# Optimization experiments

Hardware: AMD Instinct MI355X
Metric: run time of the kernel (lower is better)

## Reference

```python
import jax, jax.numpy as jnp
import numpy as np

N = 50000
E = 1600000


def gcn_conv(x, W, b, src, dst, edge_weight):
    # PyG GCNConv(normalize=False): h = x @ W.T; msg_e = h[src_e] * w_e;
    # out_i = sum_{e: dst_e = i} msg_e + bias
    h = x @ W.T                                   # [N, C_out]
    msg = h[src]                                  # [E, C_out]
    if edge_weight is not None:
        msg = msg * edge_weight[:, None]
    agg = jax.ops.segment_sum(msg, dst, num_segments=N)  # [N, C_out]
    return agg + b


def batchnorm_eval(x, gamma, beta, mean, var, eps=1e-5):
    inv = gamma * jax.lax.rsqrt(var + eps)
    return (x - mean) * inv + beta


def setup_inputs() -> dict:
    key = jax.random.key(0)
    ks = jax.random.split(key, 16)
    d = {}
    d["x"] = jax.random.normal(ks[0], (N, 128), dtype=jnp.float32)
    d["edge_index"] = jax.random.randint(ks[1], (2, E), 0, N, dtype=jnp.int64)
    d["edge_attr"] = jax.random.uniform(ks[2], (E, 8), dtype=jnp.float32)
    # layer 1: 128 -> 256, layer 2: 256 -> 256, layer 3: 256 -> 256
    s1 = 1.0 / np.sqrt(128.0)
    s2 = 1.0 / np.sqrt(256.0)
    d["W1"] = jax.random.uniform(ks[3], (256, 128), jnp.float32, -s1, s1)
    d["b1"] = jnp.zeros((256,), jnp.float32)
    d["g1"] = jnp.ones((256,), jnp.float32)
    d["beta1"] = jnp.zeros((256,), jnp.float32)
    d["m1"] = jax.random.normal(ks[4], (256,), jnp.float32) * 0.1
    d["v1"] = jax.random.uniform(ks[5], (256,), jnp.float32, minval=0.5, maxval=1.5)
    d["W2"] = jax.random.uniform(ks[6], (256, 256), jnp.float32, -s2, s2)
    d["b2"] = jnp.zeros((256,), jnp.float32)
    d["g2"] = jnp.ones((256,), jnp.float32)
    d["beta2"] = jnp.zeros((256,), jnp.float32)
    d["m2"] = jax.random.normal(ks[7], (256,), jnp.float32) * 0.1
    d["v2"] = jax.random.uniform(ks[8], (256,), jnp.float32, minval=0.5, maxval=1.5)
    d["W3"] = jax.random.uniform(ks[9], (256, 256), jnp.float32, -s2, s2)
    d["b3"] = jnp.zeros((256,), jnp.float32)
    return d


def reference(x, edge_index, edge_attr, W1, b1, g1, beta1, m1, v1,
              W2, b2, g2, beta2, m2, v2, W3, b3):
    src, dst = edge_index[0], edge_index[1]
    ew = jnp.mean(edge_attr, axis=-1)            # [E], torch.mean(edge_attr, dim=-1)
    h = gcn_conv(x, W1, b1, src, dst, ew)
    h = jax.nn.relu(batchnorm_eval(h, g1, beta1, m1, v1))
    h = gcn_conv(h, W2, b2, src, dst, ew)
    h = jax.nn.relu(batchnorm_eval(h, g2, beta2, m2, v2))
    out = gcn_conv(h, W3, b3, src, dst, None)    # last layer: no edge_weight
    return out
```

## Files before the change

kernel.cpp:

```cpp
#include <hip/hip_runtime.h>
#include <cstdint>
#include <cstddef>

#define NN 50000
#define EE 1600000
#define KB ((NN + 127) / 128)
#define PCHUNK 4096
#define SLICE 8064
#define GPAD 32

typedef __attribute__((ext_vector_type(8))) short short8;
typedef __attribute__((ext_vector_type(8))) unsigned short ushort8;
typedef __attribute__((ext_vector_type(4))) float float4v;
typedef __attribute__((ext_vector_type(2))) float floatx2;

__device__ __forceinline__ float bf2f(unsigned short u) {
    union { unsigned int i; float f; } v; v.i = ((unsigned int)u) << 16; return v.f;
}
__device__ __forceinline__ unsigned short f2bf(float f) {
    union { float f; unsigned int i; } v; v.f = f;
    unsigned int r = v.i + 0x7FFF + ((v.i >> 16) & 1);
    return (unsigned short)(r >> 16);
}

__global__ __launch_bounds__(256) void cvt_kernel(const float* __restrict__ in,
                                                  unsigned short* __restrict__ out, int n) {
    int i = (blockIdx.x * 256 + threadIdx.x) * 4;
    if (i + 3 >= n) {
        for (int k = i; k < n; k++) out[k] = f2bf(in[k]);
        return;
    }
    float4 v = *(const float4*)(in + i);
    ushort4 o;
    o.x = f2bf(v.x); o.y = f2bf(v.y); o.z = f2bf(v.z); o.w = f2bf(v.w);
    *(ushort4*)(out + i) = o;
}

__global__ __launch_bounds__(256) void cvt_w_kernel(
    const float* __restrict__ w1, unsigned short* __restrict__ o1,
    const float* __restrict__ w2, unsigned short* __restrict__ o2,
    const float* __restrict__ w3, unsigned short* __restrict__ o3)
{
    int i = (blockIdx.x * 256 + threadIdx.x) * 4;
    const float* in; unsigned short* out;
    if (i < 32768) { in = w1; out = o1; }
    else if (i < 32768 + 65536) { in = w2; out = o2; i -= 32768; }
    else { in = w3; out = o3; i -= 32768 + 65536; }
    float4 v = *(const float4*)(in + i);
    ushort4 o;
    o.x = f2bf(v.x); o.y = f2bf(v.y); o.z = f2bf(v.z); o.w = f2bf(v.w);
    *(ushort4*)(out + i) = o;
}

__global__ __launch_bounds__(256) void passA_kernel(
    const int* __restrict__ src, const int* __restrict__ dst,
    const float* __restrict__ ea, int* __restrict__ gbcnt,
    uint2* __restrict__ tmp, int E)
{
    __shared__ int bh[KB];
    __shared__ int bbase[KB];
    const int t = threadIdx.x;
    const int base_e = blockIdx.x * PCHUNK;
    for (int i = t; i < KB; i += 256) bh[i] = 0;
    __syncthreads();

    unsigned int rlo[16]; int dd[16];
    #pragma unroll
    for (int u = 0; u < 16; u++) {
        int e = base_e + u * 256 + t;
        dd[u] = -1;
        if (e < E) {
            int d = dst[e], s = src[e];
            if ((unsigned)d < NN && (unsigned)s < NN) {
                const float4* p = (const float4*)(ea + (size_t)e * 8);
                float4 a = p[0], b = p[1];
                float w = (a.x + a.y + a.z + a.w + b.x + b.y + b.z + b.w) * 0.125f;
                rlo[u] = (unsigned)s | ((unsigned)f2bf(w) << 16);
                dd[u] = d;
                atomicAdd(&bh[d >> 7], 1);
            }
        }
    }
    __syncthreads();
    for (int i = t; i < KB; i += 256) {
        int c = bh[i];
        bbase[i] = (c > 0) ? atomicAdd(&gbcnt[i * GPAD], c) : 0;
        bh[i] = 0;
    }
    __syncthreads();
    #pragma unroll
    for (int u = 0; u < 16; u++) {
        if (dd[u] >= 0) {
            int b = dd[u] >> 7;
            int pos = bbase[b] + atomicAdd(&bh[b], 1);
            if (pos < SLICE)
                tmp[(size_t)b * SLICE + pos] = (uint2){rlo[u], (unsigned)(dd[u] & 127)};
        }
    }
}

__global__ __launch_bounds__(256) void passB_kernel(
    const uint2* __restrict__ tmp, const int* __restrict__ gbcnt,
    int* __restrict__ rowptr, unsigned int* __restrict__ recs)
{
    __shared__ int cnts[KB];
    __shared__ int lh[128];
    __shared__ int lp[128];
    __shared__ int sboff;
    const int b = blockIdx.x;
    const int t = threadIdx.x;
    for (int i = t; i < KB; i += 256) cnts[i] = gbcnt[i * GPAD];
    if (t < 128) lh[t] = 0;
    __syncthreads();
    if (t == 0) {
        int s = 0;
        for (int i = 0; i < b; i++) s += cnts[i];
        sboff = s;
        if (b == KB - 1) rowptr[NN] = s + cnts[b];
    }
    __syncthreads();
    int cnt = cnts[b]; if (cnt > SLICE) cnt = SLICE;
    const uint2* slice = tmp + (size_t)b * SLICE;
    for (int i = t; i < cnt; i += 256) atomicAdd(&lh[slice[i].y], 1);
    __syncthreads();
    if (t < 128) lp[t] = lh[t];
    __syncthreads();
    #pragma unroll
    for (int off = 1; off < 128; off <<= 1) {
        int v = 0;
        if (t < 128 && t >= off) v = lp[t - off];
        __syncthreads();
        if (t < 128) lp[t] += v;
        __syncthreads();
    }
    const int node0 = b * 128;
    const int nnodes = (NN - node0 < 128) ? (NN - node0) : 128;
    if (t < nnodes) {
        int excl = lp[t] - lh[t] + sboff;
        rowptr[node0 + t] = excl;
        lh[t] = excl;
    }
    __syncthreads();
    for (int i = t; i < cnt; i += 256) {
        uint2 r = slice[i];
        int pos = atomicAdd(&lh[r.y], 1);
        recs[pos] = r.x;
    }
}

template <int C, bool HASW>
__global__ __launch_bounds__(256) void gather_bf(
    const unsigned short* __restrict__ h, const int* __restrict__ rowptr,
    const unsigned int* __restrict__ recs, unsigned short* __restrict__ agg)
{
    int node = blockIdx.x * 4 + (threadIdx.x >> 6);
    int lane = threadIdx.x & 63;
    if (node >= NN) return;
    int beg = rowptr[node], end = rowptr[node + 1];

    float a[8] = {0.f, 0.f, 0.f, 0.f, 0.f, 0.f, 0.f, 0.f};

    const int quar = lane >> 4;
    const int l16  = lane & 15;
    int j = beg;
    for (; j + 16 <= end; j += 16) {
        unsigned int r[4]; ushort8 v[4];
        #pragma unroll
        for (int u = 0; u < 4; u++) r[u] = recs[j + 4 * u + quar];
        #pragma unroll
        for (int u = 0; u < 4; u++)
            v[u] = *(const ushort8*)(h + (size_t)(r[u] & 0xFFFF) * 128 + l16 * 8);
        #pragma unroll
        for (int u = 0; u < 4; u++) {
            float w = HASW ? bf2f((unsigned short)(r[u] >> 16)) : 1.f;
            #pragma unroll
            for (int k = 0; k < 8; k++) a[k] += w * bf2f(v[u][k]);
        }
    }
    for (; j < end; j += 4) {
        int idx = j + quar;
        unsigned int r = recs[idx < end ? idx : end - 1];
        float w = (idx < end) ? (HASW ? bf2f((unsigned short)(r >> 16)) : 1.f) : 0.f;
        ushort8 v = *(const ushort8*)(h + (size_t)(r & 0xFFFF) * 128 + l16 * 8);
        #pragma unroll
        for (int k = 0; k < 8; k++) a[k] += w * bf2f(v[k]);
    }
    #pragma unroll
    for (int k = 0; k < 8; k++) {
        a[k] += __shfl_xor(a[k], 16, 64);
        a[k] += __shfl_xor(a[k], 32, 64);
    }
    if (quar == 0) {
        ushort8 o;
        #pragma unroll
        for (int k = 0; k < 8; k++) o[k] = f2bf(a[k]);
        *(ushort8*)(agg + (size_t)node * 128 + l16 * 8) = o;
    }
}

template <bool HASW>
__global__ __launch_bounds__(256) void gather_fp8(
    const unsigned char* __restrict__ h, const int* __restrict__ rowptr,
    const unsigned int* __restrict__ recs, unsigned short* __restrict__ agg)
{
    int node = blockIdx.x * 4 + (threadIdx.x >> 6);
    int lane = threadIdx.x & 63;
    if (node >= NN) return;
    int beg = rowptr[node], end = rowptr[node + 1];

    const int slot = lane >> 4;
    const int l16  = lane & 15;

    float a[16];
    #pragma unroll
    for (int k = 0; k < 16; k++) a[k] = 0.f;

    int j = beg;
    for (; j + 16 <= end; j += 16) {
        unsigned int r[4]; uint4 v[4];
        #pragma unroll
        for (int u = 0; u < 4; u++) r[u] = recs[j + 4 * u + slot];
        #pragma unroll
        for (int u = 0; u < 4; u++)
            v[u] = *(const uint4*)(h + (size_t)(r[u] & 0xFFFF) * 256 + l16 * 16);
        #pragma unroll
        for (int u = 0; u < 4; u++) {
            float w = HASW ? bf2f((unsigned short)(r[u] >> 16)) : 1.f;
            unsigned int ww[4] = {v[u].x, v[u].y, v[u].z, v[u].w};
            #pragma unroll
            for (int wi = 0; wi < 4; wi++) {
                floatx2 lo = __builtin_amdgcn_cvt_pk_f32_fp8(ww[wi], false);
                floatx2 hi = __builtin_amdgcn_cvt_pk_f32_fp8(ww[wi], true);
                a[4 * wi + 0] += w * lo.x;
                a[4 * wi + 1] += w * lo.y;
                a[4 * wi + 2] += w * hi.x;
                a[4 * wi + 3] += w * hi.y;
            }
        }
    }
    for (; j < end; j += 4) {
        int idx = j + slot;
        unsigned int r = recs[idx < end ? idx : end - 1];
        float w = (idx < end) ? (HASW ? bf2f((unsigned short)(r >> 16)) : 1.f) : 0.f;
        uint4 v = *(const uint4*)(h + (size_t)(r & 0xFFFF) * 256 + l16 * 16);
        unsigned int ww[4] = {v.x, v.y, v.z, v.w};
        #pragma unroll
        for (int wi = 0; wi < 4; wi++) {
            floatx2 lo = __builtin_amdgcn_cvt_pk_f32_fp8(ww[wi], false);
            floatx2 hi = __builtin_amdgcn_cvt_pk_f32_fp8(ww[wi], true);
            a[4 * wi + 0] += w * lo.x;
            a[4 * wi + 1] += w * lo.y;
            a[4 * wi + 2] += w * hi.x;
            a[4 * wi + 3] += w * hi.y;
        }
    }
    #pragma unroll
    for (int k = 0; k < 16; k++) {
        a[k] += __shfl_xor(a[k], 16, 64);
        a[k] += __shfl_xor(a[k], 32, 64);
    }
    if (slot == 0) {
        ushort8 o0, o1;
        #pragma unroll
        for (int k = 0; k < 8; k++) { o0[k] = f2bf(a[k]); o1[k] = f2bf(a[k + 8]); }
        *(ushort8*)(agg + (size_t)node * 256 + l16 * 16) = o0;
        *(ushort8*)(agg + (size_t)node * 256 + l16 * 16 + 8) = o1;
    }
}

template <int CIN, int MODE>
__global__ __launch_bounds__(256) void mm_mfma(
    const unsigned short* __restrict__ A, const unsigned short* __restrict__ W,
    const float* __restrict__ bias,
    const float* __restrict__ gamma, const float* __restrict__ beta,
    const float* __restrict__ mean, const float* __restrict__ var,
    void* __restrict__ out, int M)
{
    const int lane = threadIdx.x & 63;
    const int wave = threadIdx.x >> 6;
    const int quad = lane >> 4;
    const int l16  = lane & 15;
    const int row0 = blockIdx.x * 128 + (wave & 1) * 64;
    const int col0 = blockIdx.y * 128 + (wave >> 1) * 64;

    float4v acc[4][4] = {};

    for (int k0 = 0; k0 < CIN; k0 += 32) {
        const int ka = k0 + quad * 8;
        short8 af[4], bf[4];
        #pragma unroll
        for (int i = 0; i < 4; i++) {
            int r = row0 + i * 16 + l16;
            af[i] = (r < M) ? *(const short8*)(A + (size_t)r * CIN + ka) : (short8)0;
            bf[i] = *(const short8*)(W + (size_t)(col0 + i * 16 + l16) * CIN + ka);
        }
        #pragma unroll
        for (int mi = 0; mi < 4; mi++)
            #pragma unroll
            for (int ni = 0; ni < 4; ni++)
                acc[mi][ni] = __builtin_amdgcn_mfma_f32_16x16x32_bf16(
                    af[mi], bf[ni], acc[mi][ni], 0, 0, 0);
    }

    float cb[4], cmu[4], cinv[4], cbe[4];
    #pragma unroll
    for (int ni = 0; ni < 4; ni++) {
        int gc = col0 + ni * 16 + l16;
        cb[ni] = bias[gc];
        if (MODE == 1) {
            cmu[ni]  = mean[gc];
            cinv[ni] = gamma[gc] * rsqrtf(var[gc] + 1e-5f);
            cbe[ni]  = beta[gc];
        }
    }
    #pragma unroll
    for (int mi = 0; mi < 4; mi++) {
        #pragma unroll
        for (int reg = 0; reg < 4; reg++) {
            int gr = row0 + mi * 16 + quad * 4 + reg;
            if (gr >= M) continue;
            #pragma unroll
            for (int ni = 0; ni < 4; ni++) {
                int gc = col0 + ni * 16 + l16;
                float v = acc[mi][ni][reg] + cb[ni];
                if (MODE == 1) {
                    v = (v - cmu[ni]) * cinv[ni] + cbe[ni];
                    v = fmaxf(v, 0.f);
                    int pk = __builtin_amdgcn_cvt_pk_fp8_f32(v, v, 0, false);
                    ((unsigned char*)out)[(size_t)gr * 256 + gc] = (unsigned char)(pk & 0xFF);
                } else {
                    ((float*)out)[(size_t)gr * 256 + gc] = v;
                }
            }
        }
    }
}

extern "C" void kernel_launch(void* const* d_in, const int* in_sizes, int n_in,
                              void* d_out, int out_size, void* d_ws, size_t ws_size,
                              hipStream_t stream) {
    const float* x   = (const float*)d_in[0];
    const int*   ei  = (const int*)d_in[1];
    const float* ea  = (const float*)d_in[2];
    const float* W1  = (const float*)d_in[3];
    const float* b1  = (const float*)d_in[4];
    const float* g1  = (const float*)d_in[5];
    const float* be1 = (const float*)d_in[6];
    const float* m1  = (const float*)d_in[7];
    const float* v1  = (const float*)d_in[8];
    const float* W2  = (const float*)d_in[9];
    const float* b2  = (const float*)d_in[10];
    const float* g2  = (const float*)d_in[11];
    const float* be2 = (const float*)d_in[12];
    const float* m2  = (const float*)d_in[13];
    const float* v2  = (const float*)d_in[14];
    const float* W3  = (const float*)d_in[15];
    const float* b3  = (const float*)d_in[16];

    const int* src = ei;
    const int* dst = ei + EE;

    char* p = (char*)d_ws;
    auto alloc = [&](size_t bytes) { char* r = p; p += (bytes + 255) & ~255ULL; return r; };
    int*            rowptr    = (int*)alloc((NN + 1) * 4);
    int*            gbcnt     = (int*)alloc((size_t)KB * GPAD * 4);
    unsigned int*   recs      = (unsigned int*)alloc((size_t)EE * 4);
    unsigned short* xb        = (unsigned short*)alloc((size_t)NN * 128 * 2);
    unsigned short* W1b       = (unsigned short*)alloc(256 * 128 * 2);
    unsigned short* W2b       = (unsigned short*)alloc(256 * 256 * 2);
    unsigned short* W3b       = (unsigned short*)alloc(256 * 256 * 2);
    unsigned short* agg       = (unsigned short*)alloc((size_t)NN * 256 * 2);
    unsigned char*  hbuf      = (unsigned char*)alloc((size_t)NN * 256);
    float*          out       = (float*)d_out;

    uint2* tmp = (uint2*)agg;

    const int gblocks = (NN + 3) / 4;
    const int mtiles  = (NN + 127) / 128;
    const int pblocks = (EE + PCHUNK - 1) / PCHUNK;

    cvt_kernel<<<(NN * 128 / 4 + 255) / 256, 256, 0, stream>>>(x, xb, NN * 128);
    cvt_w_kernel<<<(32768 + 65536 + 65536) / 4 / 256, 256, 0, stream>>>(
        W1, W1b, W2, W2b, W3, W3b);

    hipMemsetAsync(gbcnt, 0, (size_t)KB * GPAD * 4, stream);
    passA_kernel<<<pblocks, 256, 0, stream>>>(src, dst, ea, gbcnt, tmp, EE);
    passB_kernel<<<KB, 256, 0, stream>>>(tmp, gbcnt, rowptr, recs);

    gather_bf<128, true><<<gblocks, 256, 0, stream>>>(xb, rowptr, recs, agg);
    mm_mfma<128, 1><<<dim3(mtiles, 2), 256, 0, stream>>>(
        agg, W1b, b1, g1, be1, m1, v1, hbuf, NN);

    gather_fp8<true><<<gblocks, 256, 0, stream>>>(hbuf, rowptr, recs, agg);
    mm_mfma<256, 1><<<dim3(mtiles, 2), 256, 0, stream>>>(
        agg, W2b, b2, g2, be2, m2, v2, hbuf, NN);

    gather_fp8<false><<<gblocks, 256, 0, stream>>>(hbuf, rowptr, recs, agg);
    mm_mfma<256, 0><<<dim3(mtiles, 2), 256, 0, stream>>>(
        agg, W3b, b3, nullptr, nullptr, nullptr, nullptr, out, NN);
}
```

Baseline: 459.7 us.

## Split fp8 gather into two column-half passes with 8 edges per step

The 256-channel fp8 gather now runs as two launches, each covering 128 channels (128 bytes per row). Each wave processes 8 edges in parallel with 8 lanes per edge, and the separate tail loop is replaced by predicated loads, with one extra shuffle stage for the reduction. The aim is to shrink the working set of the gathered feature table per pass so that random row reads hit L2/MALL more often, and to raise edge-level parallelism. The cost is reading the CSR records twice, launching twice, and losing row-read contiguity.

Measured after the change: 510.9 us. 11.1% more time.

```diff
diff --git a/kernel.cpp b/kernel.cpp
--- a/kernel.cpp
+++ b/kernel.cpp
@@ -148,7 +148,7 @@
     }
 }
 
-template <int C, bool HASW>
+template <bool HASW>
 __global__ __launch_bounds__(256) void gather_bf(
     const unsigned short* __restrict__ h, const int* __restrict__ rowptr,
     const unsigned int* __restrict__ recs, unsigned short* __restrict__ agg)
@@ -158,10 +158,11 @@
     if (node >= NN) return;
     int beg = rowptr[node], end = rowptr[node + 1];
 
-    float a[8] = {0.f, 0.f, 0.f, 0.f, 0.f, 0.f, 0.f, 0.f};
-
     const int quar = lane >> 4;
     const int l16  = lane & 15;
+
+    float a[8] = {0.f, 0.f, 0.f, 0.f, 0.f, 0.f, 0.f, 0.f};
+
     int j = beg;
     for (; j + 16 <= end; j += 16) {
         unsigned int r[4]; ushort8 v[4];
@@ -199,33 +200,38 @@
 }
 
 template <bool HASW>
-__global__ __launch_bounds__(256) void gather_fp8(
+__global__ __launch_bounds__(256) void gather_fp8h(
     const unsigned char* __restrict__ h, const int* __restrict__ rowptr,
-    const unsigned int* __restrict__ recs, unsigned short* __restrict__ agg)
+    const unsigned int* __restrict__ recs, unsigned short* __restrict__ agg,
+    int coff)
 {
     int node = blockIdx.x * 4 + (threadIdx.x >> 6);
     int lane = threadIdx.x & 63;
     if (node >= NN) return;
     int beg = rowptr[node], end = rowptr[node + 1];
 
-    const int slot = lane >> 4;
-    const int l16  = lane & 15;
+    const int slot = lane >> 3;
+    const int l8   = lane & 7;
 
     float a[16];
     #pragma unroll
     for (int k = 0; k < 16; k++) a[k] = 0.f;
 
-    int j = beg;
-    for (; j + 16 <= end; j += 16) {
+    const unsigned char* hb = h + coff;
+    for (int j = beg; j < end; j += 32) {
         unsigned int r[4]; uint4 v[4];
         #pragma unroll
-        for (int u = 0; u < 4; u++) r[u] = recs[j + 4 * u + slot];
+        for (int u = 0; u < 4; u++) {
+            int idx = j + 8 * u + slot;
+            r[u] = recs[idx < end ? idx : end - 1];
+        }
         #pragma unroll
         for (int u = 0; u < 4; u++)
-            v[u] = *(const uint4*)(h + (size_t)(r[u] & 0xFFFF) * 256 + l16 * 16);
+            v[u] = *(const uint4*)(hb + (size_t)(r[u] & 0xFFFF) * 256 + l8 * 16);
         #pragma unroll
         for (int u = 0; u < 4; u++) {
-            float w = HASW ? bf2f((unsigned short)(r[u] >> 16)) : 1.f;
+            int idx = j + 8 * u + slot;
+            float w = (idx < end) ? (HASW ? bf2f((unsigned short)(r[u] >> 16)) : 1.f) : 0.f;
             unsigned int ww[4] = {v[u].x, v[u].y, v[u].z, v[u].w};
             #pragma unroll
             for (int wi = 0; wi < 4; wi++) {
@@ -238,24 +244,9 @@
             }
         }
     }
-    for (; j < end; j += 4) {
-        int idx = j + slot;
-        unsigned int r = recs[idx < end ? idx : end - 1];
-        float w = (idx < end) ? (HASW ? bf2f((unsigned short)(r >> 16)) : 1.f) : 0.f;
-        uint4 v = *(const uint4*)(h + (size_t)(r & 0xFFFF) * 256 + l16 * 16);
-        unsigned int ww[4] = {v.x, v.y, v.z, v.w};
-        #pragma unroll
-        for (int wi = 0; wi < 4; wi++) {
-            floatx2 lo = __builtin_amdgcn_cvt_pk_f32_fp8(ww[wi], false);
-            floatx2 hi = __builtin_amdgcn_cvt_pk_f32_fp8(ww[wi], true);
-            a[4 * wi + 0] += w * lo.x;
-            a[4 * wi + 1] += w * lo.y;
-            a[4 * wi + 2] += w * hi.x;
-            a[4 * wi + 3] += w * hi.y;
-        }
-    }
     #pragma unroll
     for (int k = 0; k < 16; k++) {
+        a[k] += __shfl_xor(a[k], 8, 64);
         a[k] += __shfl_xor(a[k], 16, 64);
         a[k] += __shfl_xor(a[k], 32, 64);
     }
@@ -263,8 +254,9 @@
         ushort8 o0, o1;
         #pragma unroll
         for (int k = 0; k < 8; k++) { o0[k] = f2bf(a[k]); o1[k] = f2bf(a[k + 8]); }
-        *(ushort8*)(agg + (size_t)node * 256 + l16 * 16) = o0;
-        *(ushort8*)(agg + (size_t)node * 256 + l16 * 16 + 8) = o1;
+        unsigned short* dst0 = agg + (size_t)node * 256 + coff + l8 * 16;
+        *(ushort8*)(dst0) = o0;
+        *(ushort8*)(dst0 + 8) = o1;
     }
 }
 
@@ -387,15 +379,17 @@
     passA_kernel<<<pblocks, 256, 0, stream>>>(src, dst, ea, gbcnt, tmp, EE);
     passB_kernel<<<KB, 256, 0, stream>>>(tmp, gbcnt, rowptr, recs);
 
-    gather_bf<128, true><<<gblocks, 256, 0, stream>>>(xb, rowptr, recs, agg);
+    gather_bf<true><<<gblocks, 256, 0, stream>>>(xb, rowptr, recs, agg);
     mm_mfma<128, 1><<<dim3(mtiles, 2), 256, 0, stream>>>(
         agg, W1b, b1, g1, be1, m1, v1, hbuf, NN);
 
-    gather_fp8<true><<<gblocks, 256, 0, stream>>>(hbuf, rowptr, recs, agg);
+    gather_fp8h<true><<<gblocks, 256, 0, stream>>>(hbuf, rowptr, recs, agg, 0);
+    gather_fp8h<true><<<gblocks, 256, 0, stream>>>(hbuf, rowptr, recs, agg, 128);
     mm_mfma<256, 1><<<dim3(mtiles, 2), 256, 0, stream>>>(
         agg, W2b, b2, g2, be2, m2, v2, hbuf, NN);
 
-    gather_fp8<false><<<gblocks, 256, 0, stream>>>(hbuf, rowptr, recs, agg);
+    gather_fp8h<false><<<gblocks, 256, 0, stream>>>(hbuf, rowptr, recs, agg, 0);
+    gather_fp8h<false><<<gblocks, 256, 0, stream>>>(hbuf, rowptr, recs, agg, 128);
     mm_mfma<256, 0><<<dim3(mtiles, 2), 256, 0, stream>>>(
         agg, W3b, b3, nullptr, nullptr, nullptr, nullptr, out, NN);
 }
```

## Fuse neighbor gather and MFMA matmul per layer through swizzled LDS tiles

Applied to the files above, without the earlier changes.

Each layer's gather-aggregate and dense matmul are merged into one kernel. A 512-thread block aggregates 64 nodes into XOR-swizzled shared memory and then runs the MFMA matmul over all 256 output columns from LDS. This removes the global write and reread of the aggregated buffer and cuts the kernel launches from six to three. In exchange, occupancy drops because each block holds 16-32KB of LDS, and the gather inside a block is serialized per wave over 8 nodes with a sync before the matmul. Separate ping-pong activation buffers replace the reused agg/hbuf.

New measurement: 476.7 us. 1.04x slower.

```diff
diff --git a/kernel.cpp b/kernel.cpp
--- a/kernel.cpp
+++ b/kernel.cpp
@@ -8,6 +8,7 @@
 #define PCHUNK 4096
 #define SLICE 8064
 #define GPAD 32
+#define NT 782
 
 typedef __attribute__((ext_vector_type(8))) short short8;
 typedef __attribute__((ext_vector_type(8))) unsigned short ushort8;
@@ -148,154 +149,156 @@
     }
 }
 
-template <int C, bool HASW>
-__global__ __launch_bounds__(256) void gather_bf(
-    const unsigned short* __restrict__ h, const int* __restrict__ rowptr,
-    const unsigned int* __restrict__ recs, unsigned short* __restrict__ agg)
-{
-    int node = blockIdx.x * 4 + (threadIdx.x >> 6);
-    int lane = threadIdx.x & 63;
-    if (node >= NN) return;
-    int beg = rowptr[node], end = rowptr[node + 1];
-
-    float a[8] = {0.f, 0.f, 0.f, 0.f, 0.f, 0.f, 0.f, 0.f};
-
-    const int quar = lane >> 4;
-    const int l16  = lane & 15;
-    int j = beg;
-    for (; j + 16 <= end; j += 16) {
-        unsigned int r[4]; ushort8 v[4];
-        #pragma unroll
-        for (int u = 0; u < 4; u++) r[u] = recs[j + 4 * u + quar];
-        #pragma unroll
-        for (int u = 0; u < 4; u++)
-            v[u] = *(const ushort8*)(h + (size_t)(r[u] & 0xFFFF) * 128 + l16 * 8);
-        #pragma unroll
-        for (int u = 0; u < 4; u++) {
-            float w = HASW ? bf2f((unsigned short)(r[u] >> 16)) : 1.f;
-            #pragma unroll
-            for (int k = 0; k < 8; k++) a[k] += w * bf2f(v[u][k]);
-        }
-    }
-    for (; j < end; j += 4) {
-        int idx = j + quar;
-        unsigned int r = recs[idx < end ? idx : end - 1];
-        float w = (idx < end) ? (HASW ? bf2f((unsigned short)(r >> 16)) : 1.f) : 0.f;
-        ushort8 v = *(const ushort8*)(h + (size_t)(r & 0xFFFF) * 128 + l16 * 8);
-        #pragma unroll
-        for (int k = 0; k < 8; k++) a[k] += w * bf2f(v[k]);
-    }
-    #pragma unroll
-    for (int k = 0; k < 8; k++) {
-        a[k] += __shfl_xor(a[k], 16, 64);
-        a[k] += __shfl_xor(a[k], 32, 64);
-    }
-    if (quar == 0) {
-        ushort8 o;
-        #pragma unroll
-        for (int k = 0; k < 8; k++) o[k] = f2bf(a[k]);
-        *(ushort8*)(agg + (size_t)node * 128 + l16 * 8) = o;
-    }
-}
-
-template <bool HASW>
-__global__ __launch_bounds__(256) void gather_fp8(
-    const unsigned char* __restrict__ h, const int* __restrict__ rowptr,
-    const unsigned int* __restrict__ recs, unsigned short* __restrict__ agg)
-{
-    int node = blockIdx.x * 4 + (threadIdx.x >> 6);
-    int lane = threadIdx.x & 63;
-    if (node >= NN) return;
-    int beg = rowptr[node], end = rowptr[node + 1];
-
-    const int slot = lane >> 4;
-    const int l16  = lane & 15;
-
-    float a[16];
-    #pragma unroll
-    for (int k = 0; k < 16; k++) a[k] = 0.f;
-
-    int j = beg;
-    for (; j + 16 <= end; j += 16) {
-        unsigned int r[4]; uint4 v[4];
-        #pragma unroll
-        for (int u = 0; u < 4; u++) r[u] = recs[j + 4 * u + slot];
-        #pragma unroll
-        for (int u = 0; u < 4; u++)
-            v[u] = *(const uint4*)(h + (size_t)(r[u] & 0xFFFF) * 256 + l16 * 16);
-        #pragma unroll
-        for (int u = 0; u < 4; u++) {
-            float w = HASW ? bf2f((unsigned short)(r[u] >> 16)) : 1.f;
-            unsigned int ww[4] = {v[u].x, v[u].y, v[u].z, v[u].w};
-            #pragma unroll
-            for (int wi = 0; wi < 4; wi++) {
-                floatx2 lo = __builtin_amdgcn_cvt_pk_f32_fp8(ww[wi], false);
-                floatx2 hi = __builtin_amdgcn_cvt_pk_f32_fp8(ww[wi], true);
-                a[4 * wi + 0] += w * lo.x;
-                a[4 * wi + 1] += w * lo.y;
-                a[4 * wi + 2] += w * hi.x;
-                a[4 * wi + 3] += w * hi.y;
-            }
-        }
-    }
-    for (; j < end; j += 4) {
-        int idx = j + slot;
-        unsigned int r = recs[idx < end ? idx : end - 1];
-        float w = (idx < end) ? (HASW ? bf2f((unsigned short)(r >> 16)) : 1.f) : 0.f;
-        uint4 v = *(const uint4*)(h + (size_t)(r & 0xFFFF) * 256 + l16 * 16);
-        unsigned int ww[4] = {v.x, v.y, v.z, v.w};
-        #pragma unroll
-        for (int wi = 0; wi < 4; wi++) {
-            floatx2 lo = __builtin_amdgcn_cvt_pk_f32_fp8(ww[wi], false);
-            floatx2 hi = __builtin_amdgcn_cvt_pk_f32_fp8(ww[wi], true);
-            a[4 * wi + 0] += w * lo.x;
-            a[4 * wi + 1] += w * lo.y;
-            a[4 * wi + 2] += w * hi.x;
-            a[4 * wi + 3] += w * hi.y;
-        }
-    }
-    #pragma unroll
-    for (int k = 0; k < 16; k++) {
-        a[k] += __shfl_xor(a[k], 16, 64);
-        a[k] += __shfl_xor(a[k], 32, 64);
-    }
-    if (slot == 0) {
-        ushort8 o0, o1;
-        #pragma unroll
-        for (int k = 0; k < 8; k++) { o0[k] = f2bf(a[k]); o1[k] = f2bf(a[k + 8]); }
-        *(ushort8*)(agg + (size_t)node * 256 + l16 * 16) = o0;
-        *(ushort8*)(agg + (size_t)node * 256 + l16 * 16 + 8) = o1;
-    }
-}
-
-template <int CIN, int MODE>
-__global__ __launch_bounds__(256) void mm_mfma(
-    const unsigned short* __restrict__ A, const unsigned short* __restrict__ W,
+template <int CIN, int MODE, bool FP8IN>
+__global__ __launch_bounds__(512) void layer_fused(
+    const void* __restrict__ hin, const int* __restrict__ rowptr,
+    const unsigned int* __restrict__ recs, const unsigned short* __restrict__ W,
     const float* __restrict__ bias,
     const float* __restrict__ gamma, const float* __restrict__ beta,
     const float* __restrict__ mean, const float* __restrict__ var,
     void* __restrict__ out, int M)
 {
-    const int lane = threadIdx.x & 63;
-    const int wave = threadIdx.x >> 6;
+    __shared__ __align__(16) unsigned char ldsb[64 * CIN * 2];
+    const int tid  = threadIdx.x;
+    const int wave = tid >> 6;
+    const int lane = tid & 63;
+    const int node0 = blockIdx.x * 64;
+
+    if (FP8IN) {
+        const unsigned char* h = (const unsigned char*)hin;
+        const int slot = lane >> 4;
+        const int l16  = lane & 15;
+        for (int t = 0; t < 8; t++) {
+            const int lr = wave * 8 + t;
+            const int node = node0 + lr;
+            if (node >= NN) break;
+            int beg = rowptr[node], end = rowptr[node + 1];
+            float a[16];
+            #pragma unroll
+            for (int k = 0; k < 16; k++) a[k] = 0.f;
+            int j = beg;
+            for (; j + 16 <= end; j += 16) {
+                unsigned int r[4]; uint4 v[4];
+                #pragma unroll
+                for (int u = 0; u < 4; u++) r[u] = recs[j + 4 * u + slot];
+                #pragma unroll
+                for (int u = 0; u < 4; u++)
+                    v[u] = *(const uint4*)(h + (size_t)(r[u] & 0xFFFF) * 256 + l16 * 16);
+                #pragma unroll
+                for (int u = 0; u < 4; u++) {
+                    float w = bf2f((unsigned short)(r[u] >> 16));
+                    if (MODE == 0) w = 1.f;
+                    unsigned int ww[4] = {v[u].x, v[u].y, v[u].z, v[u].w};
+                    #pragma unroll
+                    for (int wi = 0; wi < 4; wi++) {
+                        floatx2 lo = __builtin_amdgcn_cvt_pk_f32_fp8(ww[wi], false);
+                        floatx2 hi = __builtin_amdgcn_cvt_pk_f32_fp8(ww[wi], true);
+                        a[4 * wi + 0] += w * lo.x;
+                        a[4 * wi + 1] += w * lo.y;
+                        a[4 * wi + 2] += w * hi.x;
+                        a[4 * wi + 3] += w * hi.y;
+                    }
+                }
+            }
+            for (; j < end; j += 4) {
+                int idx = j + slot;
+                unsigned int r = recs[idx < end ? idx : end - 1];
+                float w = (idx < end) ? ((MODE == 1) ? bf2f((unsigned short)(r >> 16)) : 1.f) : 0.f;
+                uint4 v = *(const uint4*)(h + (size_t)(r & 0xFFFF) * 256 + l16 * 16);
+                unsigned int ww[4] = {v.x, v.y, v.z, v.w};
+                #pragma unroll
+                for (int wi = 0; wi < 4; wi++) {
+                    floatx2 lo = __builtin_amdgcn_cvt_pk_f32_fp8(ww[wi], false);
+                    floatx2 hi = __builtin_amdgcn_cvt_pk_f32_fp8(ww[wi], true);
+                    a[4 * wi + 0] += w * lo.x;
+                    a[4 * wi + 1] += w * lo.y;
+                    a[4 * wi + 2] += w * hi.x;
+                    a[4 * wi + 3] += w * hi.y;
+                }
+            }
+            #pragma unroll
+            for (int k = 0; k < 16; k++) {
+                a[k] += __shfl_xor(a[k], 16, 64);
+                a[k] += __shfl_xor(a[k], 32, 64);
+            }
+            if (slot == 0) {
+                ushort8 o0, o1;
+                #pragma unroll
+                for (int k = 0; k < 8; k++) { o0[k] = f2bf(a[k]); o1[k] = f2bf(a[k + 8]); }
+                const int swz = (lr & 7) << 4;
+                *(ushort8*)(ldsb + lr * 512 + ((l16 * 32) ^ swz)) = o0;
+                *(ushort8*)(ldsb + lr * 512 + ((l16 * 32 + 16) ^ swz)) = o1;
+            }
+        }
+    } else {
+        const unsigned short* h = (const unsigned short*)hin;
+        const int quar = lane >> 4;
+        const int l16  = lane & 15;
+        for (int t = 0; t < 8; t++) {
+            const int lr = wave * 8 + t;
+            const int node = node0 + lr;
+            if (node >= NN) break;
+            int beg = rowptr[node], end = rowptr[node + 1];
+            float a[8] = {0.f, 0.f, 0.f, 0.f, 0.f, 0.f, 0.f, 0.f};
+            int j = beg;
+            for (; j + 16 <= end; j += 16) {
+                unsigned int r[4]; ushort8 v[4];
+                #pragma unroll
+                for (int u = 0; u < 4; u++) r[u] = recs[j + 4 * u + quar];
+                #pragma unroll
+                for (int u = 0; u < 4; u++)
+                    v[u] = *(const ushort8*)(h + (size_t)(r[u] & 0xFFFF) * 128 + l16 * 8);
+                #pragma unroll
+                for (int u = 0; u < 4; u++) {
+                    float w = bf2f((unsigned short)(r[u] >> 16));
+                    #pragma unroll
+                    for (int k = 0; k < 8; k++) a[k] += w * bf2f(v[u][k]);
+                }
+            }
+            for (; j < end; j += 4) {
+                int idx = j + quar;
+                unsigned int r = recs[idx < end ? idx : end - 1];
+                float w = (idx < end) ? bf2f((unsigned short)(r >> 16)) : 0.f;
+                ushort8 v = *(const ushort8*)(h + (size_t)(r & 0xFFFF) * 128 + l16 * 8);
+                #pragma unroll
+                for (int k = 0; k < 8; k++) a[k] += w * bf2f(v[k]);
+            }
+            #pragma unroll
+            for (int k = 0; k < 8; k++) {
+                a[k] += __shfl_xor(a[k], 16, 64);
+                a[k] += __shfl_xor(a[k], 32, 64);
+            }
+            if (quar == 0) {
+                ushort8 o;
+                #pragma unroll
+                for (int k = 0; k < 8; k++) o[k] = f2bf(a[k]);
+                const int swz = (lr & 7) << 4;
+                *(ushort8*)(ldsb + lr * 256 + ((l16 * 16) ^ swz)) = o;
+            }
+        }
+    }
+    __syncthreads();
+
     const int quad = lane >> 4;
     const int l16  = lane & 15;
-    const int row0 = blockIdx.x * 128 + (wave & 1) * 64;
-    const int col0 = blockIdx.y * 128 + (wave >> 1) * 64;
-
-    float4v acc[4][4] = {};
+    const int row0 = (wave & 1) * 32;
+    const int col0 = (wave >> 1) * 64;
+
+    float4v acc[2][4] = {};
 
     for (int k0 = 0; k0 < CIN; k0 += 32) {
-        const int ka = k0 + quad * 8;
-        short8 af[4], bf[4];
+        const int kb = k0 * 2 + quad * 16;
+        short8 af[2], bf[4];
         #pragma unroll
-        for (int i = 0; i < 4; i++) {
+        for (int i = 0; i < 2; i++) {
             int r = row0 + i * 16 + l16;
-            af[i] = (r < M) ? *(const short8*)(A + (size_t)r * CIN + ka) : (short8)0;
-            bf[i] = *(const short8*)(W + (size_t)(col0 + i * 16 + l16) * CIN + ka);
+            af[i] = *(const short8*)(ldsb + (size_t)r * (CIN * 2) + (kb ^ ((r & 7) << 4)));
         }
         #pragma unroll
-        for (int mi = 0; mi < 4; mi++)
+        for (int i = 0; i < 4; i++)
+            bf[i] = *(const short8*)(W + (size_t)(col0 + i * 16 + l16) * CIN + k0 + quad * 8);
+        #pragma unroll
+        for (int mi = 0; mi < 2; mi++)
             #pragma unroll
             for (int ni = 0; ni < 4; ni++)
                 acc[mi][ni] = __builtin_amdgcn_mfma_f32_16x16x32_bf16(
@@ -314,10 +317,10 @@
         }
     }
     #pragma unroll
-    for (int mi = 0; mi < 4; mi++) {
+    for (int mi = 0; mi < 2; mi++) {
         #pragma unroll
         for (int reg = 0; reg < 4; reg++) {
-            int gr = row0 + mi * 16 + quad * 4 + reg;
+            int gr = node0 + row0 + mi * 16 + quad * 4 + reg;
             if (gr >= M) continue;
             #pragma unroll
             for (int ni = 0; ni < 4; ni++) {
@@ -369,14 +372,11 @@
     unsigned short* W1b       = (unsigned short*)alloc(256 * 128 * 2);
     unsigned short* W2b       = (unsigned short*)alloc(256 * 256 * 2);
     unsigned short* W3b       = (unsigned short*)alloc(256 * 256 * 2);
-    unsigned short* agg       = (unsigned short*)alloc((size_t)NN * 256 * 2);
-    unsigned char*  hbuf      = (unsigned char*)alloc((size_t)NN * 256);
+    uint2*          tmp       = (uint2*)alloc((size_t)KB * SLICE * 8);
+    unsigned char*  hb1       = (unsigned char*)alloc((size_t)NN * 256);
+    unsigned char*  hb2       = (unsigned char*)alloc((size_t)NN * 256);
     float*          out       = (float*)d_out;
 
-    uint2* tmp = (uint2*)agg;
-
-    const int gblocks = (NN + 3) / 4;
-    const int mtiles  = (NN + 127) / 128;
     const int pblocks = (EE + PCHUNK - 1) / PCHUNK;
 
     cvt_kernel<<<(NN * 128 / 4 + 255) / 256, 256, 0, stream>>>(x, xb, NN * 128);
@@ -387,15 +387,10 @@
     passA_kernel<<<pblocks, 256, 0, stream>>>(src, dst, ea, gbcnt, tmp, EE);
     passB_kernel<<<KB, 256, 0, stream>>>(tmp, gbcnt, rowptr, recs);
 
-    gather_bf<128, true><<<gblocks, 256, 0, stream>>>(xb, rowptr, recs, agg);
-    mm_mfma<128, 1><<<dim3(mtiles, 2), 256, 0, stream>>>(
-        agg, W1b, b1, g1, be1, m1, v1, hbuf, NN);
-
-    gather_fp8<true><<<gblocks, 256, 0, stream>>>(hbuf, rowptr, recs, agg);
-    mm_mfma<256, 1><<<dim3(mtiles, 2), 256, 0, stream>>>(
-        agg, W2b, b2, g2, be2, m2, v2, hbuf, NN);
-
-    gather_fp8<false><<<gblocks, 256, 0, stream>>>(hbuf, rowptr, recs, agg);
-    mm_mfma<256, 0><<<dim3(mtiles, 2), 256, 0, stream>>>(
-        agg, W3b, b3, nullptr, nullptr, nullptr, nullptr, out, NN);
-}
+    layer_fused<128, 1, false><<<NT, 512, 0, stream>>>(
+        xb, rowptr, recs, W1b, b1, g1, be1, m1, v1, hb1, NN);
+    layer_fused<256, 1, true><<<NT, 512, 0, stream>>>(
+        hb1, rowptr, recs, W2b, b2, g2, be2, m2, v2, hb2, NN);
+    layer_fused<256, 0, true><<<NT, 512, 0, stream>>>(
+        hb2, rowptr, recs, W3b, b3, nullptr, nullptr, nullptr, nullptr, out, NN);
+}
```
